# Performance work log

Measured on AMD Instinct MI355X. Metric: run time of the kernel, lower is better.

Reference implementation:

```python
import jax, jax.numpy as jnp
import numpy as np
from jax import lax

D_MODEL = 768
D_STATE = 16
D_CONV = 4
EXPAND = 1
D_INNER = D_MODEL * EXPAND  # 768
BATCH, SEQ = 8, 4096


def setup_inputs() -> dict:
    key = jax.random.key(0)
    ks = jax.random.split(key, 8)
    s = 0.02
    x = jax.random.normal(ks[0], (BATCH, SEQ, D_MODEL), jnp.float32)
    W_in = jax.random.normal(ks[1], (D_MODEL, 2 * D_INNER), jnp.float32) * s
    conv_w = jax.random.normal(ks[2], (D_INNER, 1, D_CONV), jnp.float32) * s  # depthwise (O, I/groups=1, K)
    W_x = jax.random.normal(ks[3], (D_INNER, D_STATE + D_MODEL), jnp.float32) * s
    A_log = jax.random.normal(ks[4], (D_MODEL, D_STATE), jnp.float32)
    Dp = jnp.ones((D_MODEL,), jnp.float32)
    W_out = jax.random.normal(ks[5], (D_INNER, D_MODEL), jnp.float32) * s
    gamma = jnp.ones((D_MODEL,), jnp.float32)
    beta = jnp.zeros((D_MODEL,), jnp.float32)
    return {"x": x, "W_in": W_in, "conv_w": conv_w, "W_x": W_x,
            "A_log": A_log, "Dp": Dp, "W_out": W_out, "gamma": gamma, "beta": beta}


def _layernorm(x, gamma, beta, eps=1e-5):
    mu = x.mean(-1, keepdims=True)
    var = ((x - mu) ** 2).mean(-1, keepdims=True)
    return (x - mu) * lax.rsqrt(var + eps) * gamma + beta


def reference(x, W_in, conv_w, W_x, A_log, Dp, W_out, gamma, beta):
    residual = x
    xn = _layernorm(x, gamma, beta)
    xz = xn @ W_in                                  # (b, l, 2*d_inner)
    x1, z = jnp.split(xz, 2, axis=-1)               # each (b, l, d_inner)
    # depthwise causal conv1d (left pad d_conv-1, truncate to L == causal)
    xc = jnp.transpose(x1, (0, 2, 1))               # (b, c, l)
    xc = lax.conv_general_dilated(
        xc, conv_w, window_strides=(1,), padding=[(D_CONV - 1, 0)],
        dimension_numbers=("NCH", "OIH", "NCH"), feature_group_count=D_INNER)
    x1 = jnp.transpose(xc, (0, 2, 1))               # (b, l, d_inner)
    ssm = x1 @ W_x                                  # (b, l, d_state + d_model)
    Bm = ssm[..., :D_STATE]                         # (b, l, d_state)
    Cm = ssm[..., D_STATE:]                         # (b, l, d_model)
    A = -jnp.exp(A_log)                             # (d_model, d_state)
    # pseudo-SSM mixing (valid-einsum interpretation of the source)
    h = jnp.einsum('bln,nd->bld', x1, A) + Bm * x1.sum(-1, keepdims=True)  # (b, l, d_state)
    y = Cm * h.sum(-1, keepdims=True) + Dp * x1     # (b, l, d_inner)
    y = y * jax.nn.silu(z)
    return y @ W_out + residual
```

## Files before the change

### kernel.cpp

```cpp
#include <hip/hip_runtime.h>

typedef __bf16 bf16_t;
typedef __bf16 bf16x8 __attribute__((ext_vector_type(8)));
typedef __bf16 bf16x4 __attribute__((ext_vector_type(4)));
typedef float f32x4 __attribute__((ext_vector_type(4)));

#define DM 768
#define SEQ_LEN 4096
#define TOKENS 32768

__device__ __forceinline__ void load16_to_lds(const void* g, void* l) {
  __builtin_amdgcn_global_load_lds(
      (const __attribute__((address_space(1))) unsigned int*)g,
      (__attribute__((address_space(3))) unsigned int*)l, 16, 0, 0);
}

__global__ __launch_bounds__(256)
void prep_kernel(const float* __restrict__ W_in, const float* __restrict__ W_x,
                 const float* __restrict__ W_out, const float* __restrict__ A_log,
                 const float* __restrict__ x, const float* __restrict__ gamma,
                 const float* __restrict__ beta,
                 bf16_t* __restrict__ w_in_T, bf16_t* __restrict__ w_c_T,
                 bf16_t* __restrict__ w_out_T, float* __restrict__ a_vec,
                 float* __restrict__ b_vec, bf16_t* __restrict__ xn) {
  const int bid = blockIdx.x;
  if (bid < 4608) {
    int idx = bid * 256 + threadIdx.x;
    int n = idx / 768, k = idx - n * 768;
    w_in_T[idx] = (bf16_t)W_in[k * 1536 + n];
  } else if (bid < 6912) {
    int idx = (bid - 4608) * 256 + threadIdx.x;
    int n = idx / 768, k = idx - n * 768;
    w_c_T[idx] = (bf16_t)W_x[k * 784 + 16 + n];
  } else if (bid < 9216) {
    int idx = (bid - 6912) * 256 + threadIdx.x;
    int n = idx / 768, k = idx - n * 768;
    w_out_T[idx] = (bf16_t)W_out[k * 768 + n];
  } else if (bid < 9219) {
    int k = (bid - 9216) * 256 + threadIdx.x;
    if (k < DM) {
      float a = 0.f, b = 0.f;
#pragma unroll
      for (int d = 0; d < 16; d++) {
        a -= __expf(A_log[k * 16 + d]);
        b += W_x[(long)k * 784 + d];
      }
      a_vec[k] = a;
      b_vec[k] = b;
    }
  } else {
    const int tok = (bid - 9219) * 4 + (threadIdx.x >> 6);
    const int lane = threadIdx.x & 63;
    const float4* xr = (const float4*)(x + (long)tok * DM);
    float4 v0 = xr[lane], v1 = xr[lane + 64], v2 = xr[lane + 128];
    float s = v0.x + v0.y + v0.z + v0.w + v1.x + v1.y + v1.z + v1.w +
              v2.x + v2.y + v2.z + v2.w;
    float ss = v0.x * v0.x + v0.y * v0.y + v0.z * v0.z + v0.w * v0.w +
               v1.x * v1.x + v1.y * v1.y + v1.z * v1.z + v1.w * v1.w +
               v2.x * v2.x + v2.y * v2.y + v2.z * v2.z + v2.w * v2.w;
    for (int o = 1; o < 64; o <<= 1) { s += __shfl_xor(s, o); ss += __shfl_xor(ss, o); }
    float mu = s * (1.0f / DM);
    float var = ss * (1.0f / DM) - mu * mu;
    float inv = rsqrtf(var + 1e-5f);
    const float4* g4 = (const float4*)gamma;
    const float4* b4 = (const float4*)beta;
    bf16_t* xo = xn + (long)tok * DM;
#pragma unroll
    for (int i = 0; i < 3; i++) {
      float4 v = (i == 0) ? v0 : (i == 1) ? v1 : v2;
      float4 g = g4[lane + 64 * i], b = b4[lane + 64 * i];
      bf16x4 o;
      o[0] = (bf16_t)((v.x - mu) * inv * g.x + b.x);
      o[1] = (bf16_t)((v.y - mu) * inv * g.y + b.y);
      o[2] = (bf16_t)((v.z - mu) * inv * g.z + b.z);
      o[3] = (bf16_t)((v.w - mu) * inv * g.w + b.w);
      *(bf16x4*)(xo + lane * 4 + i * 256) = o;
    }
  }
}

__global__ __launch_bounds__(256)
void conv_kernel(const bf16_t* __restrict__ xz, const float* __restrict__ conv_w,
                 const float* __restrict__ a_vec, const float* __restrict__ b_vec,
                 bf16_t* __restrict__ x1, float* __restrict__ hs) {
  const int tok = blockIdx.x * 4 + (threadIdx.x >> 6);
  const int lane = threadIdx.x & 63;
  const int l = tok & (SEQ_LEN - 1);
  const bf16_t* base = xz + (long)tok * 1536;
  const float4* w4 = (const float4*)conv_w;
  float s = 0.f, sa = 0.f, sb = 0.f;

  {
    const int c0 = lane * 8;
    bf16x8 cur = *(const bf16x8*)(base + c0);
    bf16x8 p1 = {}, p2 = {}, p3 = {};
    if (l >= 1) p1 = *(const bf16x8*)(base + c0 - 1536);
    if (l >= 2) p2 = *(const bf16x8*)(base + c0 - 2 * 1536);
    if (l >= 3) p3 = *(const bf16x8*)(base + c0 - 3 * 1536);
    bf16x8 o;
#pragma unroll
    for (int j = 0; j < 8; j++) {
      float4 w = w4[c0 + j];
      float acc = w.w * (float)cur[j] + w.z * (float)p1[j] +
                  w.y * (float)p2[j] + w.x * (float)p3[j];
      bf16_t xb = (bf16_t)acc;
      o[j] = xb;
      float xv = (float)xb;
      s += xv; sa += xv * a_vec[c0 + j]; sb += xv * b_vec[c0 + j];
    }
    *(bf16x8*)(x1 + (long)tok * DM + c0) = o;
  }
  {
    const int c0 = 512 + lane * 4;
    bf16x4 cur = *(const bf16x4*)(base + c0);
    bf16x4 p1 = {}, p2 = {}, p3 = {};
    if (l >= 1) p1 = *(const bf16x4*)(base + c0 - 1536);
    if (l >= 2) p2 = *(const bf16x4*)(base + c0 - 2 * 1536);
    if (l >= 3) p3 = *(const bf16x4*)(base + c0 - 3 * 1536);
    bf16x4 o;
#pragma unroll
    for (int j = 0; j < 4; j++) {
      float4 w = w4[c0 + j];
      float acc = w.w * (float)cur[j] + w.z * (float)p1[j] +
                  w.y * (float)p2[j] + w.x * (float)p3[j];
      bf16_t xb = (bf16_t)acc;
      o[j] = xb;
      float xv = (float)xb;
      s += xv; sa += xv * a_vec[c0 + j]; sb += xv * b_vec[c0 + j];
    }
    *(bf16x4*)(x1 + (long)tok * DM + c0) = o;
  }
  for (int o = 1; o < 64; o <<= 1) {
    s += __shfl_xor(s, o); sa += __shfl_xor(sa, o); sb += __shfl_xor(sb, o);
  }
  if (lane == 0) hs[tok] = sa + s * sb;
}

template <int OUT_MODE>
__global__ __launch_bounds__(512, 2)
void gemm256_kernel(const bf16_t* __restrict__ A, const bf16_t* __restrict__ BT,
                    void* __restrict__ outp, const float* __restrict__ res,
                    const bf16_t* __restrict__ x1, const bf16_t* __restrict__ xz,
                    const float* __restrict__ hs, const float* __restrict__ Dp,
                    int M, int N, int K) {
  __shared__ __align__(16) bf16_t As[2][256 * 64];
  __shared__ __align__(16) bf16_t Bs[2][256 * 64];

  const int nby = N >> 8;
  const int nwg = (M >> 8) * nby;
  const int cpx = nwg >> 3;
  const int wg = blockIdx.x;
  const int swz = (wg & 7) * cpx + (wg >> 3);
  const int bx = swz / nby;
  const int by = swz - bx * nby;
  const int m0 = bx << 8;
  const int n0 = by << 8;

  const int t = threadIdx.x;
  const int lane = t & 63;
  const int wave = t >> 6;
  const int wm = (wave >> 2) * 128;
  const int wn = (wave & 3) * 64;
  const int l15 = lane & 15;
  const int quad = lane >> 4;

  const int sx0 = (((0 * 4) + quad) ^ (lane & 7)) * 8;
  const int sx1 = (((1 * 4) + quad) ^ (lane & 7)) * 8;

  const int srow = lane >> 3;
  const int scol = (((lane & 7) ^ ((lane >> 3) & 7))) * 8;

  f32x4 acc[8][4] = {};
  bf16x8 a[4][2], b0[2][2], b1[2][2];

  const bf16_t* Abase = A + (long)m0 * K + scol;
  const bf16_t* Bbase = BT + (long)n0 * K + scol;

#define STAGE_A(buf, kt) do {                                               \
    const long kk_ = (long)(kt) * 64;                                       \
    _Pragma("unroll")                                                       \
    for (int h_ = 0; h_ < 2; h_++) {                                        \
      _Pragma("unroll")                                                     \
      for (int j_ = 0; j_ < 2; j_++) {                                      \
        const int rowl_ = h_ * 128 + wave * 16 + j_ * 8;                    \
        load16_to_lds(Abase + (long)(rowl_ + srow) * K + kk_,               \
                      &As[buf][rowl_ * 64]);                                \
      } } } while (0)

#define STAGE_B(buf, kt) do {                                               \
    const long kk_ = (long)(kt) * 64;                                       \
    _Pragma("unroll")                                                       \
    for (int h_ = 0; h_ < 2; h_++) {                                        \
      _Pragma("unroll")                                                     \
      for (int j_ = 0; j_ < 2; j_++) {                                      \
        const int rowl_ = h_ * 128 + wave * 16 + j_ * 8;                    \
        load16_to_lds(Bbase + (long)(rowl_ + srow) * K + kk_,               \
                      &Bs[buf][rowl_ * 64]);                                \
      } } } while (0)

#define READ_A(qm, buf) do {                                                \
    _Pragma("unroll")                                                       \
    for (int mi_ = 0; mi_ < 4; mi_++) {                                     \
      const bf16_t* p_ = &As[buf][(wm + (qm) * 64 + mi_ * 16 + l15) * 64];  \
      a[mi_][0] = *(const bf16x8*)(p_ + sx0);                               \
      a[mi_][1] = *(const bf16x8*)(p_ + sx1);                               \
    } } while (0)

#define READ_B(dst, qn, buf) do {                                           \
    _Pragma("unroll")                                                       \
    for (int ni_ = 0; ni_ < 2; ni_++) {                                     \
      const bf16_t* p_ = &Bs[buf][(wn + (qn) * 32 + ni_ * 16 + l15) * 64];  \
      dst[ni_][0] = *(const bf16x8*)(p_ + sx0);                             \
      dst[ni_][1] = *(const bf16x8*)(p_ + sx1);                             \
    } } while (0)

#define MFMA16(qm, qn, breg) do {                                           \
    __builtin_amdgcn_s_setprio(1);                                          \
    _Pragma("unroll")                                                       \
    for (int mi_ = 0; mi_ < 4; mi_++) {                                     \
      _Pragma("unroll")                                                     \
      for (int ni_ = 0; ni_ < 2; ni_++) {                                   \
        acc[(qm) * 4 + mi_][(qn) * 2 + ni_] =                               \
            __builtin_amdgcn_mfma_f32_16x16x32_bf16(                        \
                a[mi_][0], breg[ni_][0],                                    \
                acc[(qm) * 4 + mi_][(qn) * 2 + ni_], 0, 0, 0);              \
        acc[(qm) * 4 + mi_][(qn) * 2 + ni_] =                               \
            __builtin_amdgcn_mfma_f32_16x16x32_bf16(                        \
                a[mi_][1], breg[ni_][1],                                    \
                acc[(qm) * 4 + mi_][(qn) * 2 + ni_], 0, 0, 0);              \
      } }                                                                   \
    __builtin_amdgcn_s_setprio(0);                                          \
  } while (0)

#define BAR() do { asm volatile("" ::: "memory");                           \
    __builtin_amdgcn_s_barrier();                                           \
    asm volatile("" ::: "memory"); } while (0)

  const int NT = K >> 6;
  const int NI = NT >> 1;

  STAGE_A(0, 0);
  STAGE_B(0, 0);
  STAGE_A(1, 1);
  asm volatile("s_waitcnt vmcnt(4)" ::: "memory");
  BAR();

  for (int it = 0; it < NI; ++it) {
    const int t1k = 2 * it + 1;
    const int t2k = 2 * it + 2;
    const int t3k = 2 * it + 3;
    STAGE_B(1, t1k);
    READ_A(0, 0);
    READ_B(b0, 0, 0);
    BAR();
    MFMA16(0, 0, b0);
    READ_B(b1, 1, 0);
    BAR();
    MFMA16(0, 1, b1);
    READ_A(1, 0);
    BAR();
    MFMA16(1, 1, b1);
    if (t2k < NT) STAGE_A(0, t2k);
    MFMA16(1, 0, b0);
    if (t2k < NT) { asm volatile("s_waitcnt vmcnt(4)" ::: "memory"); }
    else          { asm volatile("s_waitcnt vmcnt(0)" ::: "memory"); }
    BAR();
    if (t2k < NT) STAGE_B(0, t2k);
    READ_A(0, 1);
    READ_B(b0, 0, 1);
    BAR();
    MFMA16(0, 0, b0);
    READ_B(b1, 1, 1);
    BAR();
    MFMA16(0, 1, b1);
    READ_A(1, 1);
    BAR();
    MFMA16(1, 1, b1);
    if (t3k < NT) STAGE_A(1, t3k);
    MFMA16(1, 0, b0);
    if (t3k < NT) { asm volatile("s_waitcnt vmcnt(4)" ::: "memory"); }
    else          { asm volatile("s_waitcnt vmcnt(0)" ::: "memory"); }
    BAR();
  }

#pragma unroll
  for (int mi = 0; mi < 8; mi++) {
#pragma unroll
    for (int r = 0; r < 4; r++) {
      const int row = m0 + wm + mi * 16 + quad * 4 + r;
      float hsv = 0.f;
      if (OUT_MODE == 1) hsv = hs[row];
#pragma unroll
      for (int ni = 0; ni < 4; ni++) {
        const int col = n0 + wn + ni * 16 + l15;
        const long o = (long)row * N + col;
        float v = acc[mi][ni][r];
        if (OUT_MODE == 0) {
          ((bf16_t*)outp)[o] = (bf16_t)v;
        } else if (OUT_MODE == 1) {
          float xv = (float)x1[(long)row * DM + col];
          float zv = (float)xz[(long)row * 1536 + DM + col];
          float yv = v * hsv + Dp[col] * xv;
          yv *= zv / (1.f + __expf(-zv));
          ((bf16_t*)outp)[o] = (bf16_t)yv;
        } else {
          ((float*)outp)[o] = v + res[o];
        }
      }
    }
  }
#undef STAGE_A
#undef STAGE_B
#undef READ_A
#undef READ_B
#undef MFMA16
#undef BAR
}

template <int OUT_MODE>
__global__ __launch_bounds__(256, 3)
void gemm128_kernel(const bf16_t* __restrict__ A, const bf16_t* __restrict__ BT,
                    void* __restrict__ outp, const float* __restrict__ res,
                    const bf16_t* __restrict__ x1, const bf16_t* __restrict__ xz,
                    const float* __restrict__ hs, const float* __restrict__ Dp,
                    int M, int N, int K) {
  __shared__ __align__(16) bf16_t As[128 * 32];
  __shared__ __align__(16) bf16_t Bs[128 * 32];

  const int nby = N >> 7;
  const int nwg = (M >> 7) * nby;
  const int cpx = nwg >> 3;
  const int wg = blockIdx.x;
  const int swz = (wg & 7) * cpx + (wg >> 3);
  const int bx = swz / nby;
  const int by = swz - bx * nby;
  const int m0 = bx << 7;
  const int n0 = by << 7;

  const int t = threadIdx.x;
  const int lane = t & 63;
  const int wave = t >> 6;
  const int wm = (wave >> 1) * 64;
  const int wn = (wave & 1) * 64;
  const int l15 = lane & 15;
  const int quad = lane >> 4;

  f32x4 acc[4][4] = {};

  const int sr = lane >> 2;
  const int sc = (lane & 3) * 8;
  const bf16_t* Ag[2];
  bf16_t* lA[2];
#pragma unroll
  for (int i = 0; i < 2; i++) {
    int ch = wave * 2 + i;
    Ag[i] = A + (long)(m0 + ch * 16 + sr) * K + sc;
    lA[i] = As + ch * 512 + lane * 8;
  }
  const bf16_t* Bg[2];
  bf16_t* lB[2];
#pragma unroll
  for (int i = 0; i < 2; i++) {
    int ch = wave * 2 + i;
    Bg[i] = BT + (long)(n0 + ch * 16 + sr) * K + sc;
    lB[i] = Bs + ch * 512 + lane * 8;
  }

  for (int k0 = 0; k0 < K; k0 += 32) {
#pragma unroll
    for (int i = 0; i < 2; i++) load16_to_lds(Ag[i] + k0, lA[i]);
#pragma unroll
    for (int i = 0; i < 2; i++) load16_to_lds(Bg[i] + k0, lB[i]);
    __syncthreads();
    bf16x8 bfrag[4];
#pragma unroll
    for (int ni = 0; ni < 4; ni++)
      bfrag[ni] = *(const bf16x8*)&Bs[(wn + ni * 16 + l15) * 32 + quad * 8];
#pragma unroll
    for (int mi = 0; mi < 4; mi++) {
      bf16x8 afrag = *(const bf16x8*)&As[(wm + mi * 16 + l15) * 32 + quad * 8];
#pragma unroll
      for (int ni = 0; ni < 4; ni++)
        acc[mi][ni] = __builtin_amdgcn_mfma_f32_16x16x32_bf16(afrag, bfrag[ni], acc[mi][ni], 0, 0, 0);
    }
    __syncthreads();
  }

#pragma unroll
  for (int mi = 0; mi < 4; mi++) {
#pragma unroll
    for (int r = 0; r < 4; r++) {
      const int row = m0 + wm + mi * 16 + quad * 4 + r;
      float hsv = 0.f;
      if (OUT_MODE == 1) hsv = hs[row];
#pragma unroll
      for (int ni = 0; ni < 4; ni++) {
        const int col = n0 + wn + ni * 16 + l15;
        const long o = (long)row * N + col;
        float v = acc[mi][ni][r];
        if (OUT_MODE == 0) {
          ((bf16_t*)outp)[o] = (bf16_t)v;
        } else if (OUT_MODE == 1) {
          float xv = (float)x1[(long)row * DM + col];
          float zv = (float)xz[(long)row * 1536 + DM + col];
          float yv = v * hsv + Dp[col] * xv;
          yv *= zv / (1.f + __expf(-zv));
          ((bf16_t*)outp)[o] = (bf16_t)yv;
        } else {
          ((float*)outp)[o] = v + res[o];
        }
      }
    }
  }
}

extern "C" void kernel_launch(void* const* d_in, const int* in_sizes, int n_in,
                              void* d_out, int out_size, void* d_ws, size_t ws_size,
                              hipStream_t stream) {
  const float* x      = (const float*)d_in[0];
  const float* W_in   = (const float*)d_in[1];
  const float* conv_w = (const float*)d_in[2];
  const float* W_x    = (const float*)d_in[3];
  const float* A_log  = (const float*)d_in[4];
  const float* Dp     = (const float*)d_in[5];
  const float* W_out  = (const float*)d_in[6];
  const float* gamma  = (const float*)d_in[7];
  const float* beta   = (const float*)d_in[8];
  float* out = (float*)d_out;

  char* ws = (char*)d_ws;
  bf16_t* w_in_T  = (bf16_t*)(ws + 0);
  bf16_t* w_c_T   = (bf16_t*)(ws + 2359296);
  bf16_t* w_out_T = (bf16_t*)(ws + 3538944);
  float*  a_vec   = (float*)(ws + 4718592);
  float*  b_vec   = (float*)(ws + 4721664);
  float*  hs      = (float*)(ws + 4724736);
  bf16_t* xn      = (bf16_t*)(ws + 4855808);
  bf16_t* xz      = (bf16_t*)(ws + 55187456);
  bf16_t* x1      = (bf16_t*)(ws + 155850752);
  bf16_t* y       = xn;

  prep_kernel<<<dim3(17411), 256, 0, stream>>>(
      W_in, W_x, W_out, A_log, x, gamma, beta,
      w_in_T, w_c_T, w_out_T, a_vec, b_vec, xn);

  gemm256_kernel<0><<<dim3((TOKENS / 256) * (1536 / 256)), 512, 0, stream>>>(
      xn, w_in_T, (void*)xz, nullptr, nullptr, nullptr, nullptr, nullptr,
      TOKENS, 1536, 768);

  conv_kernel<<<dim3(TOKENS / 4), 256, 0, stream>>>(xz, conv_w, a_vec, b_vec, x1, hs);

  gemm128_kernel<1><<<dim3((TOKENS / 128) * (768 / 128)), 256, 0, stream>>>(
      x1, w_c_T, (void*)y, nullptr, x1, xz, hs, Dp,
      TOKENS, 768, 768);

  gemm128_kernel<2><<<dim3((TOKENS / 128) * (768 / 128)), 256, 0, stream>>>(
      y, w_out_T, (void*)out, x, nullptr, nullptr, nullptr, nullptr,
      TOKENS, 768, 768);
}
```

Baseline: 476.1 us.

## Replace 128x128 GEMMs with double-buffered 256x128 swizzled-LDS pipelined kernel

```diff
diff --git a/kernel.cpp b/kernel.cpp
--- a/kernel.cpp
+++ b/kernel.cpp
@@ -318,23 +318,23 @@
 }
 
 template <int OUT_MODE>
-__global__ __launch_bounds__(256, 3)
-void gemm128_kernel(const bf16_t* __restrict__ A, const bf16_t* __restrict__ BT,
-                    void* __restrict__ outp, const float* __restrict__ res,
-                    const bf16_t* __restrict__ x1, const bf16_t* __restrict__ xz,
-                    const float* __restrict__ hs, const float* __restrict__ Dp,
-                    int M, int N, int K) {
-  __shared__ __align__(16) bf16_t As[128 * 32];
-  __shared__ __align__(16) bf16_t Bs[128 * 32];
+__global__ __launch_bounds__(512, 2)
+void gemm256x128_kernel(const bf16_t* __restrict__ A, const bf16_t* __restrict__ BT,
+                        void* __restrict__ outp, const float* __restrict__ res,
+                        const bf16_t* __restrict__ x1, const bf16_t* __restrict__ xz,
+                        const float* __restrict__ hs, const float* __restrict__ Dp,
+                        int M, int N, int K) {
+  __shared__ __align__(16) bf16_t As[2][256 * 64];
+  __shared__ __align__(16) bf16_t Bs[2][128 * 64];
 
   const int nby = N >> 7;
-  const int nwg = (M >> 7) * nby;
+  const int nwg = (M >> 8) * nby;
   const int cpx = nwg >> 3;
   const int wg = blockIdx.x;
   const int swz = (wg & 7) * cpx + (wg >> 3);
   const int bx = swz / nby;
   const int by = swz - bx * nby;
-  const int m0 = bx << 7;
+  const int m0 = bx << 8;
   const int n0 = by << 7;
 
   const int t = threadIdx.x;
@@ -345,45 +345,121 @@
   const int l15 = lane & 15;
   const int quad = lane >> 4;
 
+  const int sx0 = (((0 * 4) + quad) ^ (lane & 7)) * 8;
+  const int sx1 = (((1 * 4) + quad) ^ (lane & 7)) * 8;
+
+  const int srow = lane >> 3;
+  const int scol = (((lane & 7) ^ ((lane >> 3) & 7))) * 8;
+
   f32x4 acc[4][4] = {};
-
-  const int sr = lane >> 2;
-  const int sc = (lane & 3) * 8;
-  const bf16_t* Ag[2];
-  bf16_t* lA[2];
-#pragma unroll
-  for (int i = 0; i < 2; i++) {
-    int ch = wave * 2 + i;
-    Ag[i] = A + (long)(m0 + ch * 16 + sr) * K + sc;
-    lA[i] = As + ch * 512 + lane * 8;
-  }
-  const bf16_t* Bg[2];
-  bf16_t* lB[2];
-#pragma unroll
-  for (int i = 0; i < 2; i++) {
-    int ch = wave * 2 + i;
-    Bg[i] = BT + (long)(n0 + ch * 16 + sr) * K + sc;
-    lB[i] = Bs + ch * 512 + lane * 8;
-  }
-
-  for (int k0 = 0; k0 < K; k0 += 32) {
-#pragma unroll
-    for (int i = 0; i < 2; i++) load16_to_lds(Ag[i] + k0, lA[i]);
-#pragma unroll
-    for (int i = 0; i < 2; i++) load16_to_lds(Bg[i] + k0, lB[i]);
-    __syncthreads();
-    bf16x8 bfrag[4];
-#pragma unroll
-    for (int ni = 0; ni < 4; ni++)
-      bfrag[ni] = *(const bf16x8*)&Bs[(wn + ni * 16 + l15) * 32 + quad * 8];
-#pragma unroll
-    for (int mi = 0; mi < 4; mi++) {
-      bf16x8 afrag = *(const bf16x8*)&As[(wm + mi * 16 + l15) * 32 + quad * 8];
-#pragma unroll
-      for (int ni = 0; ni < 4; ni++)
-        acc[mi][ni] = __builtin_amdgcn_mfma_f32_16x16x32_bf16(afrag, bfrag[ni], acc[mi][ni], 0, 0, 0);
-    }
-    __syncthreads();
+  bf16x8 a[2][2], b0[2][2], b1[2][2];
+
+  const bf16_t* Abase = A + (long)m0 * K + scol;
+  const bf16_t* Bbase = BT + (long)n0 * K + scol;
+
+#define S2A(buf, kt) do {                                                   \
+    const long kk_ = (long)(kt) * 64;                                       \
+    _Pragma("unroll")                                                       \
+    for (int h_ = 0; h_ < 2; h_++) {                                        \
+      _Pragma("unroll")                                                     \
+      for (int j_ = 0; j_ < 2; j_++) {                                      \
+        const int rowl_ = h_ * 128 + wave * 16 + j_ * 8;                    \
+        load16_to_lds(Abase + (long)(rowl_ + srow) * K + kk_,               \
+                      &As[buf][rowl_ * 64]);                                \
+      } } } while (0)
+
+#define S2B(buf, kt) do {                                                   \
+    const long kk_ = (long)(kt) * 64;                                       \
+    _Pragma("unroll")                                                       \
+    for (int j_ = 0; j_ < 2; j_++) {                                        \
+      const int rowl_ = wave * 16 + j_ * 8;                                 \
+      load16_to_lds(Bbase + (long)(rowl_ + srow) * K + kk_,                 \
+                    &Bs[buf][rowl_ * 64]);                                  \
+    } } while (0)
+
+#define R2A(qm, buf) do {                                                   \
+    _Pragma("unroll")                                                       \
+    for (int mi_ = 0; mi_ < 2; mi_++) {                                     \
+      const bf16_t* p_ = &As[buf][(wm + (qm) * 32 + mi_ * 16 + l15) * 64];  \
+      a[mi_][0] = *(const bf16x8*)(p_ + sx0);                               \
+      a[mi_][1] = *(const bf16x8*)(p_ + sx1);                               \
+    } } while (0)
+
+#define R2B(dst, qn, buf) do {                                              \
+    _Pragma("unroll")                                                       \
+    for (int ni_ = 0; ni_ < 2; ni_++) {                                     \
+      const bf16_t* p_ = &Bs[buf][(wn + (qn) * 32 + ni_ * 16 + l15) * 64];  \
+      dst[ni_][0] = *(const bf16x8*)(p_ + sx0);                             \
+      dst[ni_][1] = *(const bf16x8*)(p_ + sx1);                             \
+    } } while (0)
+
+#define M8(qm, qn, breg) do {                                               \
+    __builtin_amdgcn_s_setprio(1);                                          \
+    _Pragma("unroll")                                                       \
+    for (int mi_ = 0; mi_ < 2; mi_++) {                                     \
+      _Pragma("unroll")                                                     \
+      for (int ni_ = 0; ni_ < 2; ni_++) {                                   \
+        acc[(qm) * 2 + mi_][(qn) * 2 + ni_] =                               \
+            __builtin_amdgcn_mfma_f32_16x16x32_bf16(                        \
+                a[mi_][0], breg[ni_][0],                                    \
+                acc[(qm) * 2 + mi_][(qn) * 2 + ni_], 0, 0, 0);              \
+        acc[(qm) * 2 + mi_][(qn) * 2 + ni_] =                               \
+            __builtin_amdgcn_mfma_f32_16x16x32_bf16(                        \
+                a[mi_][1], breg[ni_][1],                                    \
+                acc[(qm) * 2 + mi_][(qn) * 2 + ni_], 0, 0, 0);              \
+      } }                                                                   \
+    __builtin_amdgcn_s_setprio(0);                                          \
+  } while (0)
+
+#define BAR2() do { asm volatile("" ::: "memory");                          \
+    __builtin_amdgcn_s_barrier();                                           \
+    asm volatile("" ::: "memory"); } while (0)
+
+  const int NT = K >> 6;
+  const int NI = NT >> 1;
+
+  S2A(0, 0);
+  S2B(0, 0);
+  S2A(1, 1);
+  asm volatile("s_waitcnt vmcnt(4)" ::: "memory");
+  BAR2();
+
+  for (int it = 0; it < NI; ++it) {
+    const int t1k = 2 * it + 1;
+    const int t2k = 2 * it + 2;
+    const int t3k = 2 * it + 3;
+    S2B(1, t1k);
+    R2A(0, 0);
+    R2B(b0, 0, 0);
+    BAR2();
+    M8(0, 0, b0);
+    R2B(b1, 1, 0);
+    BAR2();
+    M8(0, 1, b1);
+    R2A(1, 0);
+    BAR2();
+    M8(1, 1, b1);
+    if (t2k < NT) S2A(0, t2k);
+    M8(1, 0, b0);
+    if (t2k < NT) { asm volatile("s_waitcnt vmcnt(4)" ::: "memory"); }
+    else          { asm volatile("s_waitcnt vmcnt(0)" ::: "memory"); }
+    BAR2();
+    if (t2k < NT) S2B(0, t2k);
+    R2A(0, 1);
+    R2B(b0, 0, 1);
+    BAR2();
+    M8(0, 0, b0);
+    R2B(b1, 1, 1);
+    BAR2();
+    M8(0, 1, b1);
+    R2A(1, 1);
+    BAR2();
+    M8(1, 1, b1);
+    if (t3k < NT) S2A(1, t3k);
+    M8(1, 0, b0);
+    if (t3k < NT) { asm volatile("s_waitcnt vmcnt(4)" ::: "memory"); }
+    else          { asm volatile("s_waitcnt vmcnt(0)" ::: "memory"); }
+    BAR2();
   }
 
 #pragma unroll
@@ -412,6 +488,12 @@
       }
     }
   }
+#undef S2A
+#undef S2B
+#undef R2A
+#undef R2B
+#undef M8
+#undef BAR2
 }
 
 extern "C" void kernel_launch(void* const* d_in, const int* in_sizes, int n_in,
@@ -450,11 +532,11 @@
 
   conv_kernel<<<dim3(TOKENS / 4), 256, 0, stream>>>(xz, conv_w, a_vec, b_vec, x1, hs);
 
-  gemm128_kernel<1><<<dim3((TOKENS / 128) * (768 / 128)), 256, 0, stream>>>(
+  gemm256x128_kernel<1><<<dim3((TOKENS / 256) * (768 / 128)), 512, 0, stream>>>(
       x1, w_c_T, (void*)y, nullptr, x1, xz, hs, Dp,
       TOKENS, 768, 768);
 
-  gemm128_kernel<2><<<dim3((TOKENS / 128) * (768 / 128)), 256, 0, stream>>>(
+  gemm256x128_kernel<2><<<dim3((TOKENS / 256) * (768 / 128)), 512, 0, stream>>>(
       y, w_out_T, (void*)out, x, nullptr, nullptr, nullptr, nullptr,
       TOKENS, 768, 768);
 }
```

New measurement: 472.4 us. Within noise of the previous version (-0.8%).
